# Kernel optimization log

Measured on AMD Instinct MI355X. Metric: run time of the kernel, lower is better.

## Reference

```python
import jax, jax.numpy as jnp
import numpy as np

EPS = 1e-3  # Keras LayerNormalization default epsilon


def layernorm(x, g, b):
    mu = jnp.mean(x, axis=-1, keepdims=True)
    var = jnp.var(x, axis=-1, keepdims=True)
    return (x - mu) * jax.lax.rsqrt(var + EPS) * g + b


def setup_inputs() -> dict:
    key = jax.random.key(0)
    ks = jax.random.split(key, 16)
    B, T, C = 2, 2048, 1024
    F = 4 * C
    std = 0.02
    inp = {
        "x": jax.random.normal(ks[0], (B, T, C), jnp.float32),
        "ln1_g": jnp.ones((C,), jnp.float32),
        "ln1_b": jnp.zeros((C,), jnp.float32),
        "Wq": std * jax.random.normal(ks[1], (C, C), jnp.float32),
        "bq": jnp.zeros((C,), jnp.float32),
        "Wk": std * jax.random.normal(ks[2], (C, C), jnp.float32),
        "bk": jnp.zeros((C,), jnp.float32),
        "Wv": std * jax.random.normal(ks[3], (C, C), jnp.float32),
        "bv": jnp.zeros((C,), jnp.float32),
        "ln2_g": jnp.ones((C,), jnp.float32),
        "ln2_b": jnp.zeros((C,), jnp.float32),
        "W1": std * jax.random.normal(ks[4], (C, F), jnp.float32),
        "b1": jnp.zeros((F,), jnp.float32),
        "W2": std * jax.random.normal(ks[5], (F, C), jnp.float32),
        "b2": jnp.zeros((C,), jnp.float32),
    }
    return inp


N_HEADS = 16


def reference(x, ln1_g, ln1_b, Wq, bq, Wk, bk, Wv, bv, ln2_g, ln2_b, W1, b1, W2, b2):
    B, T, C = x.shape
    H = N_HEADS
    D = C // H

    h = layernorm(x, ln1_g, ln1_b)
    # [B,T,C] -> [B,H,T,D]
    def split_heads(y):
        return y.reshape(B, T, H, D).transpose(0, 2, 1, 3)

    q = split_heads(h @ Wq + bq)
    k = split_heads(h @ Wk + bk)
    v = split_heads(h @ Wv + bv)

    # Faithful to original: scores = K @ Q^T, i.e. scores[i,j] = k_i . q_j
    scores = jnp.einsum("bhid,bhjd->bhij", k, q) / jnp.sqrt(jnp.float32(D))
    causal = jnp.tril(jnp.ones((T, T), bool))  # [T,T]
    scores = jnp.where(causal[None, None], scores, -jnp.inf)
    w = jax.nn.softmax(scores, axis=-1)
    attn = jnp.einsum("bhij,bhjd->bhid", w, v)  # [B,H,T,D]
    attn = attn.transpose(0, 2, 1, 3).reshape(B, T, C)
    x = x + attn

    h2 = layernorm(x, ln2_g, ln2_b)
    ffn = jax.nn.gelu(h2 @ W1 + b1, approximate=False) @ W2 + b2
    x = x + ffn
    return x
```

## Files before the change

### kernel.cpp

```cpp
#include <hip/hip_runtime.h>
#include <hip/hip_bf16.h>
#include <math.h>

typedef __hip_bfloat16 bf16;
typedef __attribute__((ext_vector_type(8))) short bf16x8;
typedef __attribute__((ext_vector_type(4))) float f32x4;

__device__ __forceinline__ unsigned short f2bf_rne(float f) {
  unsigned u = __float_as_uint(f);
  u += 0x7fffu + ((u >> 16) & 1u);
  return (unsigned short)(u >> 16);
}
__device__ __forceinline__ float bf2f(unsigned short s) {
  return __uint_as_float(((unsigned)s) << 16);
}

__device__ __forceinline__ float gelu_fast(float v) {
  float u = v * (0.7978845608f + 0.0356774081f * v * v);
  float t = __builtin_amdgcn_exp2f(u * 2.8853900818f);
  float r = __builtin_amdgcn_rcpf(t + 1.0f);
  return v - v * r;
}

#define GLOBAL_AS __attribute__((address_space(1)))
#define LDS_AS __attribute__((address_space(3)))
__device__ __forceinline__ void gl2lds16(const void* g, void* l) {
  __builtin_amdgcn_global_load_lds((const GLOBAL_AS void*)g, (LDS_AS void*)l, 16, 0, 0);
}

__global__ __launch_bounds__(256) void ln_kernel(const float* __restrict__ x,
                                                 const float* __restrict__ g,
                                                 const float* __restrict__ b,
                                                 bf16* __restrict__ h) {
  int row = blockIdx.x, t = threadIdx.x;
  const float4 xv = ((const float4*)(x + (size_t)row * 1024))[t];
  float s = xv.x + xv.y + xv.z + xv.w;
  float sq = xv.x * xv.x + xv.y * xv.y + xv.z * xv.z + xv.w * xv.w;
  #pragma unroll
  for (int m = 1; m < 64; m <<= 1) { s += __shfl_xor(s, m); sq += __shfl_xor(sq, m); }
  __shared__ float ps[4], pq[4];
  if ((t & 63) == 0) { ps[t >> 6] = s; pq[t >> 6] = sq; }
  __syncthreads();
  s = ps[0] + ps[1] + ps[2] + ps[3];
  sq = pq[0] + pq[1] + pq[2] + pq[3];
  float mean = s * (1.0f / 1024.0f);
  float var = sq * (1.0f / 1024.0f) - mean * mean;
  float rs = rsqrtf(var + 1e-3f);
  float4 gv = ((const float4*)g)[t];
  float4 bv = ((const float4*)b)[t];
  ushort4 o;
  o.x = f2bf_rne((xv.x - mean) * rs * gv.x + bv.x);
  o.y = f2bf_rne((xv.y - mean) * rs * gv.y + bv.y);
  o.z = f2bf_rne((xv.z - mean) * rs * gv.z + bv.z);
  o.w = f2bf_rne((xv.w - mean) * rs * gv.w + bv.w);
  ((ushort4*)(h + (size_t)row * 1024))[t] = o;
}

__device__ __forceinline__ void tr_tile(const float* __restrict__ W, bf16* __restrict__ WT,
                                        int R, int Cc, int bx, int by, int t) {
  __shared__ float tile[32][33];
  int tx = t & 31, ty = t >> 5;
  #pragma unroll
  for (int k = 0; k < 4; k++) {
    int rr = ty + k * 8;
    tile[rr][tx] = W[(size_t)(by + rr) * Cc + bx + tx];
  }
  __syncthreads();
  unsigned short* out = reinterpret_cast<unsigned short*>(WT);
  #pragma unroll
  for (int k = 0; k < 4; k++) {
    int rr = ty + k * 8;
    out[(size_t)(bx + rr) * R + by + tx] = f2bf_rne(tile[tx][rr]);
  }
}

__global__ __launch_bounds__(256) void transpose_all(const float* __restrict__ Wq,
                                                     const float* __restrict__ Wk,
                                                     const float* __restrict__ Wv,
                                                     const float* __restrict__ W1,
                                                     const float* __restrict__ W2,
                                                     bf16* __restrict__ WqkT,
                                                     bf16* __restrict__ W1T,
                                                     bf16* __restrict__ W2T) {
  int id = blockIdx.x, t = threadIdx.x;
  if (id < 3072) {
    int sect = id >> 10, r = id & 1023;
    const float* W = sect == 0 ? Wq : (sect == 1 ? Wk : Wv);
    bf16* WT = WqkT + (size_t)sect * 1048576;
    tr_tile(W, WT, 1024, 1024, (r & 31) * 32, (r >> 5) * 32, t);
  } else if (id < 7168) {
    int r = id - 3072;
    tr_tile(W1, W1T, 1024, 4096, (r & 127) * 32, (r >> 7) * 32, t);
  } else {
    int r = id - 7168;
    tr_tile(W2, W2T, 4096, 1024, (r & 31) * 32, (r >> 5) * 32, t);
  }
}

__device__ __forceinline__ void kloop_bk64(const bf16* __restrict__ A,
                                           const bf16* __restrict__ BT,
                                           int K, int kbeg, int kend, int m0, int n0,
                                           int wave, int lane,
                                           bf16 (*As)[64], bf16 (*Bs)[64],
                                           f32x4 acc[4][4]) {
  int lrow = lane & 15, quad = lane >> 4;
  int wm = (wave >> 1) * 64, wn = (wave & 1) * 64;
  int srow = wave * 32 + (lane >> 3);
  int gsw = ((lane & 7) ^ (lane >> 3)) * 8;
  int sw = lrow & 7;
  for (int k0 = kbeg; k0 < kend; k0 += 64) {
    __syncthreads();
    #pragma unroll
    for (int j = 0; j < 4; j++) {
      int row = srow + j * 8;
      gl2lds16(A + (size_t)(m0 + row) * K + k0 + gsw, (char*)As + wave * 4096 + j * 1024);
      gl2lds16(BT + (size_t)(n0 + row) * K + k0 + gsw, (char*)Bs + wave * 4096 + j * 1024);
    }
    __syncthreads();
    bf16x8 af[2][4], bfr[2][4];
    #pragma unroll
    for (int h = 0; h < 2; h++) {
      #pragma unroll
      for (int i = 0; i < 4; i++)
        af[h][i] = *(const bf16x8*)((const char*)&As[wm + i * 16 + lrow][0] +
                                    (((h * 4 + quad) ^ sw) * 16));
      #pragma unroll
      for (int j = 0; j < 4; j++)
        bfr[h][j] = *(const bf16x8*)((const char*)&Bs[wn + j * 16 + lrow][0] +
                                     (((h * 4 + quad) ^ sw) * 16));
    }
    #pragma unroll
    for (int h = 0; h < 2; h++)
      #pragma unroll
      for (int i = 0; i < 4; i++)
        #pragma unroll
        for (int j = 0; j < 4; j++)
          acc[i][j] = __builtin_amdgcn_mfma_f32_16x16x32_bf16(af[h][i], bfr[h][j], acc[i][j], 0, 0, 0);
  }
}

__global__ __launch_bounds__(256) void gemm_ffn1(const bf16* __restrict__ A,
                                                 const bf16* __restrict__ BT,
                                                 const float* __restrict__ bias,
                                                 bf16* __restrict__ out,
                                                 int N, int K) {
  __shared__ bf16 As[128][64];
  __shared__ bf16 Bs[128][64];
  int t = threadIdx.x;
  int n0 = blockIdx.x * 128, m0 = blockIdx.y * 128;
  int lane = t & 63, wave = t >> 6;
  f32x4 acc[4][4];
  #pragma unroll
  for (int i = 0; i < 4; i++)
    #pragma unroll
    for (int j = 0; j < 4; j++) acc[i][j] = (f32x4){0.f, 0.f, 0.f, 0.f};
  kloop_bk64(A, BT, K, 0, K, m0, n0, wave, lane, As, Bs, acc);

  int wm = (wave >> 1) * 64, wn = (wave & 1) * 64;
  int r4 = (lane >> 4) * 4, cl = lane & 15;
  unsigned short* os = reinterpret_cast<unsigned short*>(out);
  #pragma unroll
  for (int i = 0; i < 4; i++)
    #pragma unroll
    for (int j = 0; j < 4; j++) {
      int col = n0 + wn + j * 16 + cl;
      float bval = bias[col];
      #pragma unroll
      for (int r = 0; r < 4; r++) {
        int row = m0 + wm + i * 16 + r4 + r;
        os[(size_t)row * N + col] = f2bf_rne(gelu_fast(acc[i][j][r] + bval));
      }
    }
}

__global__ __launch_bounds__(256) void gemm_ffn2_sk(const bf16* __restrict__ A,
                                                    const bf16* __restrict__ BT,
                                                    unsigned short* __restrict__ p0,
                                                    unsigned short* __restrict__ p1,
                                                    int K) {
  __shared__ bf16 As[128][64];
  __shared__ bf16 Bs[128][64];
  int t = threadIdx.x;
  int n0 = blockIdx.x * 128, m0 = blockIdx.y * 128;
  int z = blockIdx.z;
  int lane = t & 63, wave = t >> 6;
  f32x4 acc[4][4];
  #pragma unroll
  for (int i = 0; i < 4; i++)
    #pragma unroll
    for (int j = 0; j < 4; j++) acc[i][j] = (f32x4){0.f, 0.f, 0.f, 0.f};
  kloop_bk64(A, BT, K, z * 2048, z * 2048 + 2048, m0, n0, wave, lane, As, Bs, acc);

  unsigned short* p = z ? p1 : p0;
  int wm = (wave >> 1) * 64, wn = (wave & 1) * 64;
  int r4 = (lane >> 4) * 4, cl = lane & 15;
  #pragma unroll
  for (int i = 0; i < 4; i++)
    #pragma unroll
    for (int j = 0; j < 4; j++) {
      int col = n0 + wn + j * 16 + cl;
      #pragma unroll
      for (int r = 0; r < 4; r++) {
        int row = m0 + wm + i * 16 + r4 + r;
        p[(size_t)row * 1024 + col] = f2bf_rne(acc[i][j][r]);
      }
    }
}

__global__ __launch_bounds__(256) void reduce_ffn2(const unsigned short* __restrict__ p0,
                                                   const unsigned short* __restrict__ p1,
                                                   const float* __restrict__ x1,
                                                   const float* __restrict__ bias,
                                                   float* __restrict__ out) {
  int row = blockIdx.x, t = threadIdx.x;
  size_t base = (size_t)row * 1024;
  ushort4 a = ((const ushort4*)(p0 + base))[t];
  ushort4 b = ((const ushort4*)(p1 + base))[t];
  float4 xv = ((const float4*)(x1 + base))[t];
  float4 bv = ((const float4*)bias)[t];
  float4 o;
  o.x = bf2f(a.x) + bf2f(b.x) + xv.x + bv.x;
  o.y = bf2f(a.y) + bf2f(b.y) + xv.y + bv.y;
  o.z = bf2f(a.z) + bf2f(b.z) + xv.z + bv.z;
  o.w = bf2f(a.w) + bf2f(b.w) + xv.w + bv.w;
  ((float4*)(out + base))[t] = o;
}

__global__ __launch_bounds__(256) void gemm_qkv(const bf16* __restrict__ A,
                                                const bf16* __restrict__ BT,
                                                const float* __restrict__ bq,
                                                const float* __restrict__ bk,
                                                const float* __restrict__ bv,
                                                bf16* __restrict__ qb,
                                                bf16* __restrict__ kb,
                                                bf16* __restrict__ vt,
                                                int K) {
  __shared__ bf16 As[128][64];
  __shared__ bf16 Bs[128][64];
  int t = threadIdx.x;
  int n0 = blockIdx.x * 128, m0 = blockIdx.y * 128;
  int lane = t & 63, wave = t >> 6;
  f32x4 acc[4][4];
  #pragma unroll
  for (int i = 0; i < 4; i++)
    #pragma unroll
    for (int j = 0; j < 4; j++) acc[i][j] = (f32x4){0.f, 0.f, 0.f, 0.f};
  kloop_bk64(A, BT, K, 0, K, m0, n0, wave, lane, As, Bs, acc);

  int sect = n0 >> 10;
  const float* bias = sect == 0 ? bq : (sect == 1 ? bk : bv);
  int wm = (wave >> 1) * 64, wn = (wave & 1) * 64;
  int r4 = (lane >> 4) * 4, cl = lane & 15;
  #pragma unroll
  for (int i = 0; i < 4; i++)
    #pragma unroll
    for (int j = 0; j < 4; j++) {
      int col = n0 + wn + j * 16 + cl;
      int c1 = col & 1023;
      float bval = bias[c1];
      int row0 = m0 + wm + i * 16 + r4;
      if (sect < 2) {
        bf16* o = sect == 0 ? qb : kb;
        unsigned short* os = reinterpret_cast<unsigned short*>(o);
        #pragma unroll
        for (int r = 0; r < 4; r++)
          os[(size_t)(row0 + r) * 1024 + c1] = f2bf_rne(acc[i][j][r] + bval);
      } else {
        int hh = c1 >> 6, d = c1 & 63;
        int b = row0 >> 11, t0 = row0 & 2047;
        ushort4 pk;
        pk.x = f2bf_rne(acc[i][j][0] + bval);
        pk.y = f2bf_rne(acc[i][j][1] + bval);
        pk.z = f2bf_rne(acc[i][j][2] + bval);
        pk.w = f2bf_rne(acc[i][j][3] + bval);
        *(ushort4*)((unsigned short*)vt + (size_t)((b * 16 + hh) * 64 + d) * 2048 + t0) = pk;
      }
    }
}

__global__ __launch_bounds__(256) void attn_mfma(const bf16* __restrict__ qb,
                                                 const bf16* __restrict__ kb,
                                                 const bf16* __restrict__ vt,
                                                 const float* __restrict__ x,
                                                 float* __restrict__ x1) {
  __shared__ bf16 QP[64][72];
  __shared__ bf16 KV[2][2][64][64];
  int t = threadIdx.x;
  int bh = blockIdx.x;
  int b = bh >> 4, h = bh & 15;
  size_t qk_base = (size_t)b * 2048 * 1024 + (size_t)h * 64;
  size_t vt_base = (size_t)bh * 64 * 2048;
  int lane = t & 63, wave = t >> 6;
  int l = lane & 15, quad = lane >> 4;
  int sw = l & 7;
  int srow8 = lane >> 3;
  int scol = ((lane & 7) ^ srow8) * 8;
  const float cs = 0.125f * 1.44269504088896f;
  int y = blockIdx.y;

  for (int pass = 0; pass < 2; pass++) {
    int it = pass ? 31 - y : y;
    int i0 = it * 64;
    int njt = it + 1;
    __syncthreads();
    #pragma unroll
    for (int c0 = 0; c0 < 512; c0 += 256) {
      int c = c0 + t;
      int row = c >> 3, col8 = (c & 7) * 8;
      *(uint4*)&QP[row][col8] = *(const uint4*)(kb + qk_base + (size_t)(i0 + row) * 1024 + col8);
    }
    #pragma unroll
    for (int c = 0; c < 2; c++) {
      int rr = wave * 16 + c * 8 + srow8;
      gl2lds16(qb + qk_base + (size_t)rr * 1024 + scol,
               (char*)KV + wave * 2048 + c * 1024);
      gl2lds16(vt + vt_base + (size_t)rr * 2048 + scol,
               (char*)KV + 8192 + wave * 2048 + c * 1024);
    }
    __syncthreads();

    bf16x8 qf0 = *(const bf16x8*)&QP[wave * 16 + l][quad * 8];
    bf16x8 qf1 = *(const bf16x8*)&QP[wave * 16 + l][32 + quad * 8];
    float lsum = 0.f;
    f32x4 Oacc[4];
    #pragma unroll
    for (int dt = 0; dt < 4; dt++) Oacc[dt] = (f32x4){0.f, 0.f, 0.f, 0.f};
    int iblk = i0 + wave * 16;

    int buf = 0;
    for (int jt = 0; jt < njt; jt++) {
      int j0v = jt * 64;
      if (jt + 1 < njt) {
        int j1 = j0v + 64;
        #pragma unroll
        for (int c = 0; c < 2; c++) {
          int rr = wave * 16 + c * 8 + srow8;
          gl2lds16(qb + qk_base + (size_t)(j1 + rr) * 1024 + scol,
                   (char*)KV + (buf ^ 1) * 16384 + wave * 2048 + c * 1024);
          gl2lds16(vt + vt_base + (size_t)rr * 2048 + j1 + scol,
                   (char*)KV + (buf ^ 1) * 16384 + 8192 + wave * 2048 + c * 1024);
        }
      }

      const bf16* Kb = &KV[buf][0][0][0];
      #pragma unroll
      for (int nt = 0; nt < 4; nt++) {
        int jb = j0v + nt * 16;
        uint2 pk;
        if (jb > iblk + 15) {
          pk.x = 0u; pk.y = 0u;
        } else {
          const bf16* kr = Kb + (nt * 16 + l) * 64;
          bf16x8 kf0 = *(const bf16x8*)(kr + ((quad ^ sw) * 8));
          bf16x8 kf1 = *(const bf16x8*)(kr + (((4 + quad) ^ sw) * 8));
          f32x4 sv = (f32x4){0.f, 0.f, 0.f, 0.f};
          sv = __builtin_amdgcn_mfma_f32_16x16x32_bf16(kf0, qf0, sv, 0, 0, 0);
          sv = __builtin_amdgcn_mfma_f32_16x16x32_bf16(kf1, qf1, sv, 0, 0, 0);
          float p0, p1, p2, p3;
          if (jb + 15 <= iblk) {
            p0 = __builtin_amdgcn_exp2f(sv[0] * cs);
            p1 = __builtin_amdgcn_exp2f(sv[1] * cs);
            p2 = __builtin_amdgcn_exp2f(sv[2] * cs);
            p3 = __builtin_amdgcn_exp2f(sv[3] * cs);
          } else {
            int i_ = iblk + l, jbase = jb + quad * 4;
            p0 = (jbase + 0 > i_) ? 0.f : __builtin_amdgcn_exp2f(sv[0] * cs);
            p1 = (jbase + 1 > i_) ? 0.f : __builtin_amdgcn_exp2f(sv[1] * cs);
            p2 = (jbase + 2 > i_) ? 0.f : __builtin_amdgcn_exp2f(sv[2] * cs);
            p3 = (jbase + 3 > i_) ? 0.f : __builtin_amdgcn_exp2f(sv[3] * cs);
          }
          lsum += (p0 + p1) + (p2 + p3);
          union { __hip_bfloat162 h2; unsigned u; } c0u, c1u;
          c0u.h2 = __float22bfloat162_rn(make_float2(p0, p1));
          c1u.h2 = __float22bfloat162_rn(make_float2(p2, p3));
          pk.x = c0u.u; pk.y = c1u.u;
        }
        *(uint2*)&QP[wave * 16 + l][nt * 16 + quad * 4] = pk;
      }
      asm volatile("s_waitcnt lgkmcnt(0)" ::: "memory");

      bf16x8 ap0 = *(const bf16x8*)&QP[wave * 16 + l][quad * 8];
      bf16x8 ap1 = *(const bf16x8*)&QP[wave * 16 + l][32 + quad * 8];
      const bf16* Vb = &KV[buf][1][0][0];
      #pragma unroll
      for (int dt = 0; dt < 4; dt++) {
        const bf16* vr = Vb + (dt * 16 + l) * 64;
        bf16x8 bv0 = *(const bf16x8*)(vr + ((quad ^ sw) * 8));
        bf16x8 bv1 = *(const bf16x8*)(vr + (((4 + quad) ^ sw) * 8));
        Oacc[dt] = __builtin_amdgcn_mfma_f32_16x16x32_bf16(ap0, bv0, Oacc[dt], 0, 0, 0);
        Oacc[dt] = __builtin_amdgcn_mfma_f32_16x16x32_bf16(ap1, bv1, Oacc[dt], 0, 0, 0);
      }
      __syncthreads();
      buf ^= 1;
    }

    lsum += __shfl_xor(lsum, 16);
    lsum += __shfl_xor(lsum, 32);
    #pragma unroll
    for (int r = 0; r < 4; r++) {
      float lv = __shfl(lsum, quad * 4 + r);
      float inv = 1.0f / lv;
      int row = i0 + wave * 16 + quad * 4 + r;
      size_t gi = qk_base + (size_t)row * 1024;
      #pragma unroll
      for (int dt = 0; dt < 4; dt++) {
        int d = dt * 16 + l;
        x1[gi + d] = x[gi + d] + Oacc[dt][r] * inv;
      }
    }
  }
}

extern "C" void kernel_launch(void* const* d_in, const int* in_sizes, int n_in,
                              void* d_out, int out_size, void* d_ws, size_t ws_size,
                              hipStream_t stream) {
  const float* x    = (const float*)d_in[0];
  const float* ln1g = (const float*)d_in[1];
  const float* ln1b = (const float*)d_in[2];
  const float* Wq   = (const float*)d_in[3];
  const float* bq   = (const float*)d_in[4];
  const float* Wk   = (const float*)d_in[5];
  const float* bk   = (const float*)d_in[6];
  const float* Wv   = (const float*)d_in[7];
  const float* bv   = (const float*)d_in[8];
  const float* ln2g = (const float*)d_in[9];
  const float* ln2b = (const float*)d_in[10];
  const float* W1   = (const float*)d_in[11];
  const float* b1   = (const float*)d_in[12];
  const float* W2   = (const float*)d_in[13];
  const float* b2   = (const float*)d_in[14];

  char* ws = (char*)d_ws;
  float* x1  = (float*)(ws + 0);
  bf16* h    = (bf16*)(ws + 16777216);
  bf16* WqkT = (bf16*)(ws + 25165824);
  bf16* W1T  = (bf16*)(ws + 31457280);
  bf16* W2T  = (bf16*)(ws + 39845888);
  bf16* qb   = (bf16*)(ws + 48234496);
  bf16* kb   = (bf16*)(ws + 56623104);
  bf16* vt   = (bf16*)(ws + 65011712);
  bf16* act  = (bf16*)(ws + 73400320);

  transpose_all<<<11264, 256, 0, stream>>>(Wq, Wk, Wv, W1, W2, WqkT, W1T, W2T);
  ln_kernel<<<4096, 256, 0, stream>>>(x, ln1g, ln1b, h);
  gemm_qkv<<<dim3(24, 32), 256, 0, stream>>>(h, WqkT, bq, bk, bv, qb, kb, vt, 1024);
  attn_mfma<<<dim3(32, 16), 256, 0, stream>>>(qb, kb, vt, x, x1);
  ln_kernel<<<4096, 256, 0, stream>>>(x1, ln2g, ln2b, h);
  gemm_ffn1<<<dim3(32, 32), 256, 0, stream>>>(h, W1T, b1, act, 4096, 1024);
  gemm_ffn2_sk<<<dim3(8, 32, 2), 256, 0, stream>>>(act, W2T,
      (unsigned short*)qb, (unsigned short*)kb, 4096);
  reduce_ffn2<<<4096, 256, 0, stream>>>((const unsigned short*)qb, (const unsigned short*)kb,
                                        x1, b2, (float*)d_out);
}
```

Measured before the change: 321.3 us.

## Use 256x256 double-buffered pipelined GEMM mainloop for QKV and FFN1

Adds a new mainloop that computes a 256x256 output tile with 512 threads and 128KB of dynamic LDS. It double-buffers global-to-LDS loads and interleaves them with the MFMA phases, using explicit barriers, waitcnt and setprio. Only the QKV and FFN1 GEMMs move to it; the split-K FFN2 keeps the old 128x128 loop. The larger tiles raise data reuse per byte loaded and hide load latency. In exchange the grids are much smaller (192 and 256 blocks), which may underfill the CUs, and the hand-written barrier sequencing adds risk.

```diff
diff --git a/kernel.cpp b/kernel.cpp
--- a/kernel.cpp
+++ b/kernel.cpp
@@ -97,73 +97,132 @@
   }
 }
 
-__device__ __forceinline__ void kloop_bk64(const bf16* __restrict__ A,
-                                           const bf16* __restrict__ BT,
-                                           int K, int kbeg, int kend, int m0, int n0,
-                                           int wave, int lane,
-                                           bf16 (*As)[64], bf16 (*Bs)[64],
-                                           f32x4 acc[4][4]) {
-  int lrow = lane & 15, quad = lane >> 4;
-  int wm = (wave >> 1) * 64, wn = (wave & 1) * 64;
-  int srow = wave * 32 + (lane >> 3);
-  int gsw = ((lane & 7) ^ (lane >> 3)) * 8;
-  int sw = lrow & 7;
-  for (int k0 = kbeg; k0 < kend; k0 += 64) {
-    __syncthreads();
+__device__ __forceinline__ void mainloop_256(const bf16* __restrict__ A,
+                                             const bf16* __restrict__ BT,
+                                             int K, int m0, int n0,
+                                             char* ldsb, int t,
+                                             f32x4 (&acc)[8][4]) {
+  const int lane = t & 63, wave = t >> 6;
+  const int l = lane & 15, quad = lane >> 4;
+  const int wm = (wave >> 2) * 128, wn = (wave & 3) * 64;
+  const int srow = wave * 8 + (lane >> 3);
+  const int scol = ((lane & 7) ^ (lane >> 3)) * 8;
+  const int grp0 = (quad ^ (l & 7)) * 16;
+  const int grp1 = ((4 + quad) ^ (l & 7)) * 16;
+
+  bf16x8 a[4][2], b01[2][2], b23[2][2];
+
+  auto stA = [&](int buf, int half, int kt) {
+    const bf16* s = A + (size_t)(m0 + half * 128 + srow) * K + kt * 64 + scol;
+    char* d = ldsb + buf * 65536 + half * 16384 + wave * 1024;
+    gl2lds16(s, d);
+    gl2lds16(s + (size_t)64 * K, d + 8192);
+  };
+  auto stB = [&](int buf, int half, int kt) {
+    const bf16* s = BT + (size_t)(n0 + half * 128 + srow) * K + kt * 64 + scol;
+    char* d = ldsb + buf * 65536 + 32768 + half * 16384 + wave * 1024;
+    gl2lds16(s, d);
+    gl2lds16(s + (size_t)64 * K, d + 8192);
+  };
+  auto rdA = [&](int buf, int mh) {
+    const char* base = ldsb + buf * 65536 + (wm + mh * 64 + l) * 128;
+    #pragma unroll
+    for (int ii = 0; ii < 4; ii++) {
+      a[ii][0] = *(const bf16x8*)(base + ii * 2048 + grp0);
+      a[ii][1] = *(const bf16x8*)(base + ii * 2048 + grp1);
+    }
+  };
+  auto rdB = [&](int buf, int nh, bf16x8 (&bb)[2][2]) {
+    const char* base = ldsb + buf * 65536 + 32768 + (wn + nh * 32 + l) * 128;
+    #pragma unroll
+    for (int jj = 0; jj < 2; jj++) {
+      bb[jj][0] = *(const bf16x8*)(base + jj * 2048 + grp0);
+      bb[jj][1] = *(const bf16x8*)(base + jj * 2048 + grp1);
+    }
+  };
+  auto mm4 = [&](int mi, bf16x8 (&bb)[2][2], int nj) {
+    #pragma unroll
+    for (int ii = 0; ii < 4; ii++)
+      #pragma unroll
+      for (int jj = 0; jj < 2; jj++) {
+        acc[mi + ii][nj + jj] = __builtin_amdgcn_mfma_f32_16x16x32_bf16(
+            a[ii][0], bb[jj][0], acc[mi + ii][nj + jj], 0, 0, 0);
+        acc[mi + ii][nj + jj] = __builtin_amdgcn_mfma_f32_16x16x32_bf16(
+            a[ii][1], bb[jj][1], acc[mi + ii][nj + jj], 0, 0, 0);
+      }
+  };
+
+#define BARX() __builtin_amdgcn_s_barrier()
+#define LGKM0() do { asm volatile("s_waitcnt lgkmcnt(0)" ::: "memory"); \
+                     __builtin_amdgcn_sched_barrier(0); } while (0)
+#define HALF4(BC, DOA, SAB, SAK, DOB, SBB, SBK, VMN)                      \
+  do {                                                                    \
+    rdA(BC, 0); rdB(BC, 0, b01);                                          \
+    if (DOA) stA(SAB, 0, SAK);                                            \
+    BARX(); LGKM0();                                                      \
+    __builtin_amdgcn_s_setprio(1); mm4(0, b01, 0);                        \
+    __builtin_amdgcn_s_setprio(0); BARX();                                \
+    rdB(BC, 1, b23);                                                      \
+    if (DOA) stA(SAB, 1, SAK);                                            \
+    BARX(); LGKM0();                                                      \
+    __builtin_amdgcn_s_setprio(1); mm4(0, b23, 2);                        \
+    __builtin_amdgcn_s_setprio(0); BARX();                                \
+    rdA(BC, 1);                                                           \
+    if (DOB) stB(SBB, 0, SBK);                                            \
+    BARX(); LGKM0();                                                      \
+    __builtin_amdgcn_s_setprio(1); mm4(4, b01, 0);                        \
+    __builtin_amdgcn_s_setprio(0); BARX();                                \
+    if (DOB) stB(SBB, 1, SBK);                                            \
+    BARX();                                                               \
+    __builtin_amdgcn_s_setprio(1); mm4(4, b23, 2);                        \
+    __builtin_amdgcn_s_setprio(0);                                        \
+    asm volatile("s_waitcnt vmcnt(" VMN ")" ::: "memory");                \
+    BARX();                                                               \
+  } while (0)
+
+  const int nt = K >> 6;
+  stA(0, 0, 0); stA(0, 1, 0);
+  stB(0, 0, 0); stB(0, 1, 0);
+  stB(1, 0, 1); stB(1, 1, 1);
+  asm volatile("s_waitcnt vmcnt(4)" ::: "memory");
+  BARX();
+  int tt = 0;
+  for (; tt + 2 < nt; tt += 2) {
+    HALF4(0, 1, 1, tt + 1, 1, 0, tt + 2, "4");
+    HALF4(1, 1, 0, tt + 2, 1, 1, tt + 3, "4");
+  }
+  HALF4(0, 1, 1, tt + 1, 0, 0, 0, "0");
+  HALF4(1, 0, 0, 0, 0, 0, 0, "0");
+#undef HALF4
+#undef LGKM0
+#undef BARX
+}
+
+__global__ __launch_bounds__(512, 2) void gemm_ffn1(const bf16* __restrict__ A,
+                                                    const bf16* __restrict__ BT,
+                                                    const float* __restrict__ bias,
+                                                    bf16* __restrict__ out,
+                                                    int N, int K) {
+  extern __shared__ char lds[];
+  int t = threadIdx.x;
+  int n0 = blockIdx.x * 256, m0 = blockIdx.y * 256;
+  f32x4 acc[8][4];
+  #pragma unroll
+  for (int i = 0; i < 8; i++)
+    #pragma unroll
+    for (int j = 0; j < 4; j++) acc[i][j] = (f32x4){0.f, 0.f, 0.f, 0.f};
+  mainloop_256(A, BT, K, m0, n0, lds, t, acc);
+
+  int lane = t & 63, wave = t >> 6;
+  int l = lane & 15, quad = lane >> 4;
+  int wm = (wave >> 2) * 128, wn = (wave & 3) * 64;
+  int r4 = quad * 4;
+  unsigned short* os = reinterpret_cast<unsigned short*>(out);
+  #pragma unroll
+  for (int i = 0; i < 8; i++)
     #pragma unroll
     for (int j = 0; j < 4; j++) {
-      int row = srow + j * 8;
-      gl2lds16(A + (size_t)(m0 + row) * K + k0 + gsw, (char*)As + wave * 4096 + j * 1024);
-      gl2lds16(BT + (size_t)(n0 + row) * K + k0 + gsw, (char*)Bs + wave * 4096 + j * 1024);
-    }
-    __syncthreads();
-    bf16x8 af[2][4], bfr[2][4];
-    #pragma unroll
-    for (int h = 0; h < 2; h++) {
-      #pragma unroll
-      for (int i = 0; i < 4; i++)
-        af[h][i] = *(const bf16x8*)((const char*)&As[wm + i * 16 + lrow][0] +
-                                    (((h * 4 + quad) ^ sw) * 16));
-      #pragma unroll
-      for (int j = 0; j < 4; j++)
-        bfr[h][j] = *(const bf16x8*)((const char*)&Bs[wn + j * 16 + lrow][0] +
-                                     (((h * 4 + quad) ^ sw) * 16));
-    }
-    #pragma unroll
-    for (int h = 0; h < 2; h++)
-      #pragma unroll
-      for (int i = 0; i < 4; i++)
-        #pragma unroll
-        for (int j = 0; j < 4; j++)
-          acc[i][j] = __builtin_amdgcn_mfma_f32_16x16x32_bf16(af[h][i], bfr[h][j], acc[i][j], 0, 0, 0);
-  }
-}
-
-__global__ __launch_bounds__(256) void gemm_ffn1(const bf16* __restrict__ A,
-                                                 const bf16* __restrict__ BT,
-                                                 const float* __restrict__ bias,
-                                                 bf16* __restrict__ out,
-                                                 int N, int K) {
-  __shared__ bf16 As[128][64];
-  __shared__ bf16 Bs[128][64];
-  int t = threadIdx.x;
-  int n0 = blockIdx.x * 128, m0 = blockIdx.y * 128;
-  int lane = t & 63, wave = t >> 6;
-  f32x4 acc[4][4];
-  #pragma unroll
-  for (int i = 0; i < 4; i++)
-    #pragma unroll
-    for (int j = 0; j < 4; j++) acc[i][j] = (f32x4){0.f, 0.f, 0.f, 0.f};
-  kloop_bk64(A, BT, K, 0, K, m0, n0, wave, lane, As, Bs, acc);
-
-  int wm = (wave >> 1) * 64, wn = (wave & 1) * 64;
-  int r4 = (lane >> 4) * 4, cl = lane & 15;
-  unsigned short* os = reinterpret_cast<unsigned short*>(out);
-  #pragma unroll
-  for (int i = 0; i < 4; i++)
-    #pragma unroll
-    for (int j = 0; j < 4; j++) {
-      int col = n0 + wn + j * 16 + cl;
+      int col = n0 + wn + j * 16 + l;
       float bval = bias[col];
       #pragma unroll
       for (int r = 0; r < 4; r++) {
@@ -173,89 +232,36 @@
     }
 }
 
-__global__ __launch_bounds__(256) void gemm_ffn2_sk(const bf16* __restrict__ A,
-                                                    const bf16* __restrict__ BT,
-                                                    unsigned short* __restrict__ p0,
-                                                    unsigned short* __restrict__ p1,
-                                                    int K) {
-  __shared__ bf16 As[128][64];
-  __shared__ bf16 Bs[128][64];
+__global__ __launch_bounds__(512, 2) void gemm_qkv(const bf16* __restrict__ A,
+                                                   const bf16* __restrict__ BT,
+                                                   const float* __restrict__ bq,
+                                                   const float* __restrict__ bk,
+                                                   const float* __restrict__ bv,
+                                                   bf16* __restrict__ qb,
+                                                   bf16* __restrict__ kb,
+                                                   bf16* __restrict__ vt,
+                                                   int K) {
+  extern __shared__ char lds[];
   int t = threadIdx.x;
-  int n0 = blockIdx.x * 128, m0 = blockIdx.y * 128;
-  int z = blockIdx.z;
+  int n0 = blockIdx.x * 256, m0 = blockIdx.y * 256;
+  f32x4 acc[8][4];
+  #pragma unroll
+  for (int i = 0; i < 8; i++)
+    #pragma unroll
+    for (int j = 0; j < 4; j++) acc[i][j] = (f32x4){0.f, 0.f, 0.f, 0.f};
+  mainloop_256(A, BT, K, m0, n0, lds, t, acc);
+
   int lane = t & 63, wave = t >> 6;
-  f32x4 acc[4][4];
-  #pragma unroll
-  for (int i = 0; i < 4; i++)
-    #pragma unroll
-    for (int j = 0; j < 4; j++) acc[i][j] = (f32x4){0.f, 0.f, 0.f, 0.f};
-  kloop_bk64(A, BT, K, z * 2048, z * 2048 + 2048, m0, n0, wave, lane, As, Bs, acc);
-
-  unsigned short* p = z ? p1 : p0;
-  int wm = (wave >> 1) * 64, wn = (wave & 1) * 64;
-  int r4 = (lane >> 4) * 4, cl = lane & 15;
-  #pragma unroll
-  for (int i = 0; i < 4; i++)
-    #pragma unroll
-    for (int j = 0; j < 4; j++) {
-      int col = n0 + wn + j * 16 + cl;
-      #pragma unroll
-      for (int r = 0; r < 4; r++) {
-        int row = m0 + wm + i * 16 + r4 + r;
-        p[(size_t)row * 1024 + col] = f2bf_rne(acc[i][j][r]);
-      }
-    }
-}
-
-__global__ __launch_bounds__(256) void reduce_ffn2(const unsigned short* __restrict__ p0,
-                                                   const unsigned short* __restrict__ p1,
-                                                   const float* __restrict__ x1,
-                                                   const float* __restrict__ bias,
-                                                   float* __restrict__ out) {
-  int row = blockIdx.x, t = threadIdx.x;
-  size_t base = (size_t)row * 1024;
-  ushort4 a = ((const ushort4*)(p0 + base))[t];
-  ushort4 b = ((const ushort4*)(p1 + base))[t];
-  float4 xv = ((const float4*)(x1 + base))[t];
-  float4 bv = ((const float4*)bias)[t];
-  float4 o;
-  o.x = bf2f(a.x) + bf2f(b.x) + xv.x + bv.x;
-  o.y = bf2f(a.y) + bf2f(b.y) + xv.y + bv.y;
-  o.z = bf2f(a.z) + bf2f(b.z) + xv.z + bv.z;
-  o.w = bf2f(a.w) + bf2f(b.w) + xv.w + bv.w;
-  ((float4*)(out + base))[t] = o;
-}
-
-__global__ __launch_bounds__(256) void gemm_qkv(const bf16* __restrict__ A,
-                                                const bf16* __restrict__ BT,
-                                                const float* __restrict__ bq,
-                                                const float* __restrict__ bk,
-                                                const float* __restrict__ bv,
-                                                bf16* __restrict__ qb,
-                                                bf16* __restrict__ kb,
-                                                bf16* __restrict__ vt,
-                                                int K) {
-  __shared__ bf16 As[128][64];
-  __shared__ bf16 Bs[128][64];
-  int t = threadIdx.x;
-  int n0 = blockIdx.x * 128, m0 = blockIdx.y * 128;
-  int lane = t & 63, wave = t >> 6;
-  f32x4 acc[4][4];
-  #pragma unroll
-  for (int i = 0; i < 4; i++)
-    #pragma unroll
-    for (int j = 0; j < 4; j++) acc[i][j] = (f32x4){0.f, 0.f, 0.f, 0.f};
-  kloop_bk64(A, BT, K, 0, K, m0, n0, wave, lane, As, Bs, acc);
-
+  int l = lane & 15, quad = lane >> 4;
+  int wm = (wave >> 2) * 128, wn = (wave & 3) * 64;
   int sect = n0 >> 10;
   const float* bias = sect == 0 ? bq : (sect == 1 ? bk : bv);
-  int wm = (wave >> 1) * 64, wn = (wave & 1) * 64;
-  int r4 = (lane >> 4) * 4, cl = lane & 15;
-  #pragma unroll
-  for (int i = 0; i < 4; i++)
+  int r4 = quad * 4;
+  #pragma unroll
+  for (int i = 0; i < 8; i++)
     #pragma unroll
     for (int j = 0; j < 4; j++) {
-      int col = n0 + wn + j * 16 + cl;
+      int col = n0 + wn + j * 16 + l;
       int c1 = col & 1023;
       float bval = bias[c1];
       int row0 = m0 + wm + i * 16 + r4;
@@ -276,6 +282,101 @@
         *(ushort4*)((unsigned short*)vt + (size_t)((b * 16 + hh) * 64 + d) * 2048 + t0) = pk;
       }
     }
+}
+
+__device__ __forceinline__ void kloop_bk64(const bf16* __restrict__ A,
+                                           const bf16* __restrict__ BT,
+                                           int K, int kbeg, int kend, int m0, int n0,
+                                           int wave, int lane,
+                                           bf16 (*As)[64], bf16 (*Bs)[64],
+                                           f32x4 acc[4][4]) {
+  int lrow = lane & 15, quad = lane >> 4;
+  int wm = (wave >> 1) * 64, wn = (wave & 1) * 64;
+  int srow = wave * 32 + (lane >> 3);
+  int gsw = ((lane & 7) ^ (lane >> 3)) * 8;
+  int sw = lrow & 7;
+  for (int k0 = kbeg; k0 < kend; k0 += 64) {
+    __syncthreads();
+    #pragma unroll
+    for (int j = 0; j < 4; j++) {
+      int row = srow + j * 8;
+      gl2lds16(A + (size_t)(m0 + row) * K + k0 + gsw, (char*)As + wave * 4096 + j * 1024);
+      gl2lds16(BT + (size_t)(n0 + row) * K + k0 + gsw, (char*)Bs + wave * 4096 + j * 1024);
+    }
+    __syncthreads();
+    bf16x8 af[2][4], bfr[2][4];
+    #pragma unroll
+    for (int h = 0; h < 2; h++) {
+      #pragma unroll
+      for (int i = 0; i < 4; i++)
+        af[h][i] = *(const bf16x8*)((const char*)&As[wm + i * 16 + lrow][0] +
+                                    (((h * 4 + quad) ^ sw) * 16));
+      #pragma unroll
+      for (int j = 0; j < 4; j++)
+        bfr[h][j] = *(const bf16x8*)((const char*)&Bs[wn + j * 16 + lrow][0] +
+                                     (((h * 4 + quad) ^ sw) * 16));
+    }
+    #pragma unroll
+    for (int h = 0; h < 2; h++)
+      #pragma unroll
+      for (int i = 0; i < 4; i++)
+        #pragma unroll
+        for (int j = 0; j < 4; j++)
+          acc[i][j] = __builtin_amdgcn_mfma_f32_16x16x32_bf16(af[h][i], bfr[h][j], acc[i][j], 0, 0, 0);
+  }
+}
+
+__global__ __launch_bounds__(256) void gemm_ffn2_sk(const bf16* __restrict__ A,
+                                                    const bf16* __restrict__ BT,
+                                                    unsigned short* __restrict__ p0,
+                                                    unsigned short* __restrict__ p1,
+                                                    int K) {
+  __shared__ bf16 As[128][64];
+  __shared__ bf16 Bs[128][64];
+  int t = threadIdx.x;
+  int n0 = blockIdx.x * 128, m0 = blockIdx.y * 128;
+  int z = blockIdx.z;
+  int lane = t & 63, wave = t >> 6;
+  f32x4 acc[4][4];
+  #pragma unroll
+  for (int i = 0; i < 4; i++)
+    #pragma unroll
+    for (int j = 0; j < 4; j++) acc[i][j] = (f32x4){0.f, 0.f, 0.f, 0.f};
+  kloop_bk64(A, BT, K, z * 2048, z * 2048 + 2048, m0, n0, wave, lane, As, Bs, acc);
+
+  unsigned short* p = z ? p1 : p0;
+  int wm = (wave >> 1) * 64, wn = (wave & 1) * 64;
+  int r4 = (lane >> 4) * 4, cl = lane & 15;
+  #pragma unroll
+  for (int i = 0; i < 4; i++)
+    #pragma unroll
+    for (int j = 0; j < 4; j++) {
+      int col = n0 + wn + j * 16 + cl;
+      #pragma unroll
+      for (int r = 0; r < 4; r++) {
+        int row = m0 + wm + i * 16 + r4 + r;
+        p[(size_t)row * 1024 + col] = f2bf_rne(acc[i][j][r]);
+      }
+    }
+}
+
+__global__ __launch_bounds__(256) void reduce_ffn2(const unsigned short* __restrict__ p0,
+                                                   const unsigned short* __restrict__ p1,
+                                                   const float* __restrict__ x1,
+                                                   const float* __restrict__ bias,
+                                                   float* __restrict__ out) {
+  int row = blockIdx.x, t = threadIdx.x;
+  size_t base = (size_t)row * 1024;
+  ushort4 a = ((const ushort4*)(p0 + base))[t];
+  ushort4 b = ((const ushort4*)(p1 + base))[t];
+  float4 xv = ((const float4*)(x1 + base))[t];
+  float4 bv = ((const float4*)bias)[t];
+  float4 o;
+  o.x = bf2f(a.x) + bf2f(b.x) + xv.x + bv.x;
+  o.y = bf2f(a.y) + bf2f(b.y) + xv.y + bv.y;
+  o.z = bf2f(a.z) + bf2f(b.z) + xv.z + bv.z;
+  o.w = bf2f(a.w) + bf2f(b.w) + xv.w + bv.w;
+  ((float4*)(out + base))[t] = o;
 }
 
 __global__ __launch_bounds__(256) void attn_mfma(const bf16* __restrict__ qb,
@@ -441,12 +542,21 @@
   bf16* vt   = (bf16*)(ws + 65011712);
   bf16* act  = (bf16*)(ws + 73400320);
 
+  static bool s_attr_done = false;
+  if (!s_attr_done) {
+    hipFuncSetAttribute(reinterpret_cast<const void*>(gemm_qkv),
+                        hipFuncAttributeMaxDynamicSharedMemorySize, 131072);
+    hipFuncSetAttribute(reinterpret_cast<const void*>(gemm_ffn1),
+                        hipFuncAttributeMaxDynamicSharedMemorySize, 131072);
+    s_attr_done = true;
+  }
+
   transpose_all<<<11264, 256, 0, stream>>>(Wq, Wk, Wv, W1, W2, WqkT, W1T, W2T);
   ln_kernel<<<4096, 256, 0, stream>>>(x, ln1g, ln1b, h);
-  gemm_qkv<<<dim3(24, 32), 256, 0, stream>>>(h, WqkT, bq, bk, bv, qb, kb, vt, 1024);
+  gemm_qkv<<<dim3(12, 16), 512, 131072, stream>>>(h, WqkT, bq, bk, bv, qb, kb, vt, 1024);
   attn_mfma<<<dim3(32, 16), 256, 0, stream>>>(qb, kb, vt, x, x1);
   ln_kernel<<<4096, 256, 0, stream>>>(x1, ln2g, ln2b, h);
-  gemm_ffn1<<<dim3(32, 32), 256, 0, stream>>>(h, W1T, b1, act, 4096, 1024);
+  gemm_ffn1<<<dim3(16, 16), 512, 131072, stream>>>(h, W1T, b1, act, 4096, 1024);
   gemm_ffn2_sk<<<dim3(8, 32, 2), 256, 0, stream>>>(act, W2T,
       (unsigned short*)qb, (unsigned short*)kb, 4096);
   reduce_ffn2<<<4096, 256, 0, stream>>>((const unsigned short*)qb, (const unsigned short*)kb,
```

Result: faster. 304.2 us (-5.3%).
